# Optimization experiments

Hardware: AMD Instinct MI355X
Metric: run time of the kernel (lower is better)

The kernel has to match this reference:

```python
import jax, jax.numpy as jnp
import numpy as np

NEG_SLOPE = 0.2
EPS = 1e-16

def gatv2(x, edge_index, edge_attr, Wl, bl, We, att, bias):
    """PyG GATv2Conv, heads=1, share_weights=True, with edge_dim."""
    N = x.shape[0]
    h = x @ Wl + bl                      # [N, out] shared lin_l == lin_r
    src, dst = edge_index[0], edge_index[1]
    hj = h[src]                          # source (message) features [E, out]
    hi = h[dst]                          # target features [E, out]
    e = jax.nn.leaky_relu(hi + hj + edge_attr @ We, NEG_SLOPE)  # [E, out]
    score = e @ att                      # [E]
    # segment softmax over edges grouped by destination node
    smax = jax.ops.segment_max(score, dst, num_segments=N)
    ex = jnp.exp(score - smax[dst])
    denom = jax.ops.segment_sum(ex, dst, num_segments=N)
    alpha = ex / (denom[dst] + EPS)      # [E]
    out = jax.ops.segment_sum(hj * alpha[:, None], dst, num_segments=N)
    return out + bias


def setup_inputs() -> dict:
    key = jax.random.key(0)
    N, E = 50000, 800000
    D_IN, D_LAT, D_EDGE, N_ACT = 128, 128, 16, 32
    ks = jax.random.split(key, 16)
    s = 0.05
    inp = {
        "x": jax.random.normal(ks[0], (N, D_IN), jnp.float32),
        "edge_index": jax.random.randint(ks[1], (2, E), 0, N, jnp.int32),
        "edge_attr": jax.random.normal(ks[2], (E, D_EDGE), jnp.float32),
        # gnn_layer: D_IN -> D_LAT
        "Wl1": jax.random.normal(ks[3], (D_IN, D_LAT), jnp.float32) * s,
        "bl1": jnp.zeros((D_LAT,), jnp.float32),
        "We1": jax.random.normal(ks[4], (D_EDGE, D_LAT), jnp.float32) * s,
        "att1": jax.random.normal(ks[5], (D_LAT,), jnp.float32) * s,
        "bias1": jnp.zeros((D_LAT,), jnp.float32),
        # node_layer: D_LAT -> 1
        "Wl2": jax.random.normal(ks[6], (D_LAT, 1), jnp.float32) * s,
        "bl2": jnp.zeros((1,), jnp.float32),
        "We2": jax.random.normal(ks[7], (D_EDGE, 1), jnp.float32) * s,
        "att2": jax.random.normal(ks[8], (1,), jnp.float32) * s,
        "bias2": jnp.zeros((1,), jnp.float32),
        # action_layer: D_LAT -> N_ACT
        "Wl3": jax.random.normal(ks[9], (D_LAT, N_ACT), jnp.float32) * s,
        "bl3": jnp.zeros((N_ACT,), jnp.float32),
        "We3": jax.random.normal(ks[10], (D_EDGE, N_ACT), jnp.float32) * s,
        "att3": jax.random.normal(ks[11], (N_ACT,), jnp.float32) * s,
        "bias3": jnp.zeros((N_ACT,), jnp.float32),
    }
    return inp


def reference(x, edge_index, edge_attr,
              Wl1, bl1, We1, att1, bias1,
              Wl2, bl2, We2, att2, bias2,
              Wl3, bl3, We3, att3, bias3):
    latent = gatv2(x, edge_index, edge_attr, Wl1, bl1, We1, att1, bias1)          # [N, D_LAT]
    node_logits = gatv2(latent, edge_index, edge_attr, Wl2, bl2, We2, att2, bias2)[:, 0]  # [N]
    action_logits = gatv2(latent, edge_index, edge_attr, Wl3, bl3, We3, att3, bias3)      # [N, A]
    # categorical sampling with fixed key (deterministic reference)
    k1, k2 = jax.random.split(jax.random.key(42))
    node_sel = jax.random.categorical(k1, node_logits)
    node_lp = jax.nn.log_softmax(node_logits)[node_sel]
    act_logits_sel = action_logits[node_sel, :]
    action_sel = jax.random.categorical(k2, act_logits_sel)
    action_lp = jax.nn.log_softmax(act_logits_sel)[action_sel]
    return (node_sel, action_sel, node_lp + action_lp)
```

## Files before the change

kernel.cpp:

```cpp
#include <hip/hip_runtime.h>
#include <stdint.h>
#include <math.h>

#define NEG 0.2f
#define TINYF 1.1754943508222875e-38f

typedef float f4 __attribute__((ext_vector_type(4)));
typedef float f2 __attribute__((ext_vector_type(2)));

__host__ __device__ inline void threefry2x32(uint32_t k0, uint32_t k1,
                                             uint32_t x0, uint32_t x1,
                                             uint32_t* o0, uint32_t* o1) {
  uint32_t ks0 = k0, ks1 = k1, ks2 = k0 ^ k1 ^ 0x1BD11BDAu;
  x0 += ks0; x1 += ks1;
#define RR(r) { x0 += x1; x1 = (x1 << (r)) | (x1 >> (32 - (r))); x1 ^= x0; }
  RR(13) RR(15) RR(26) RR(6)
  x0 += ks1; x1 += ks2 + 1u;
  RR(17) RR(29) RR(16) RR(24)
  x0 += ks2; x1 += ks0 + 2u;
  RR(13) RR(15) RR(26) RR(6)
  x0 += ks0; x1 += ks1 + 3u;
  RR(17) RR(29) RR(16) RR(24)
  x0 += ks1; x1 += ks2 + 4u;
  RR(13) RR(15) RR(26) RR(6)
  x0 += ks2; x1 += ks0 + 5u;
#undef RR
  *o0 = x0; *o1 = x1;
}

__device__ inline float gumbel_part(uint32_t ka, uint32_t kb, uint32_t i) {
  uint32_t o0, o1;
  threefry2x32(ka, kb, 0u, i, &o0, &o1);
  uint32_t bits = o0 ^ o1;
  float f = __uint_as_float((bits >> 9) | 0x3f800000u) - 1.0f;
  float u = fmaxf(TINYF, f + TINYF);
  return -logf(-logf(u));
}

__global__ void count_kernel(const int* __restrict__ ei, int E, int* __restrict__ counts) {
  int e = blockIdx.x * blockDim.x + threadIdx.x;
  if (e < E) atomicAdd(&counts[ei[E + e]], 1);
}

#define SCB 256
__global__ __launch_bounds__(256) void scan_partial_kernel(const int* __restrict__ counts,
    int N, int chunk, int* __restrict__ bsum) {
  int b = blockIdx.x;
  int s0 = b * chunk, s1 = s0 + chunk; if (s1 > N) s1 = N;
  int tid = threadIdx.x;
  int v = 0;
  for (int i = s0 + tid; i < s1; i += 256) v += counts[i];
  __shared__ int red[256];
  red[tid] = v; __syncthreads();
  for (int s = 128; s; s >>= 1) { if (tid < s) red[tid] += red[tid + s]; __syncthreads(); }
  if (tid == 0) bsum[b] = red[0];
}

__global__ __launch_bounds__(256) void scan_offsets_kernel(const int* __restrict__ bsum,
    int* __restrict__ boff, int* __restrict__ row_start, int N) {
  int tid = threadIdx.x; int lane = tid & 63; int wv = tid >> 6;
  __shared__ int wsum[4];
  int v = bsum[tid];
  int incl = v;
#pragma unroll
  for (int off = 1; off < 64; off <<= 1) {
    int t = __shfl_up(incl, off);
    if (lane >= off) incl += t;
  }
  if (lane == 63) wsum[wv] = incl;
  __syncthreads();
  if (tid == 0) {
    int s = 0;
    for (int k = 0; k < 4; k++) { int t = wsum[k]; wsum[k] = s; s += t; }
    row_start[N] = s;
  }
  __syncthreads();
  boff[tid] = wsum[wv] + incl - v;
}

__global__ __launch_bounds__(256) void scan_apply_kernel(const int* __restrict__ counts,
    const int* __restrict__ boff, int N, int chunk,
    int* __restrict__ row_start, int* __restrict__ cursor) {
  int b = blockIdx.x;
  int s0 = b * chunk, s1 = s0 + chunk; if (s1 > N) s1 = N;
  int tid = threadIdx.x; int lane = tid & 63; int wv = tid >> 6;
  __shared__ int wsum[4];
  __shared__ int tot_s;
  __shared__ int base_s;
  if (tid == 0) base_s = boff[b];
  __syncthreads();
  for (int c0 = s0; c0 < s1; c0 += 256) {
    int i = c0 + tid;
    int v = (i < s1) ? counts[i] : 0;
    int incl = v;
#pragma unroll
    for (int off = 1; off < 64; off <<= 1) {
      int t = __shfl_up(incl, off);
      if (lane >= off) incl += t;
    }
    if (lane == 63) wsum[wv] = incl;
    __syncthreads();
    if (tid == 0) {
      int s = 0;
      for (int k = 0; k < 4; k++) { int t = wsum[k]; wsum[k] = s; s += t; }
      tot_s = s;
    }
    __syncthreads();
    int base = base_s;
    int excl = base + wsum[wv] + incl - v;
    if (i < s1) { row_start[i] = excl; cursor[i] = excl; }
    __syncthreads();
    if (tid == 0) base_s = base + tot_s;
    __syncthreads();
  }
}

__global__ void scatter_kernel(const int* __restrict__ ei, const float* __restrict__ ea,
                               int E, int* __restrict__ cursor,
                               int* __restrict__ src_csr, float* __restrict__ ea_csr) {
  int e = blockIdx.x * blockDim.x + threadIdx.x;
  if (e < E) {
    int d = ei[E + e];
    int p = atomicAdd(&cursor[d], 1);
    src_csr[p] = ei[e];
    const float4* s4 = (const float4*)&ea[(size_t)e * 16];
    float4* d4 = (float4*)&ea_csr[(size_t)p * 16];
    float4 t0 = s4[0], t1 = s4[1], t2 = s4[2], t3 = s4[3];
    d4[0] = t0; d4[1] = t1; d4[2] = t2; d4[3] = t3;
  }
}

__global__ __launch_bounds__(256) void gemm128_kernel(const float* __restrict__ X,
    const float* __restrict__ W, const float* __restrict__ bias,
    float* __restrict__ out, int M) {
  __shared__ float xs[128][33];
  int row0 = blockIdx.x * 32;
  int tid = threadIdx.x;
  for (int idx = tid; idx < 32 * 128; idx += 256) {
    int r = idx >> 7;
    int k = idx & 127;
    int row = row0 + r;
    xs[k][r] = (row < M) ? X[(size_t)row * 128 + k] : 0.0f;
  }
  __syncthreads();
  int tc = tid & 31, tr = tid >> 5;
  int c0 = tc * 4, r0 = tr * 4;
  float acc[4][4] = {};
#pragma unroll 4
  for (int k = 0; k < 128; k++) {
    float4 w = *(const float4*)&W[k * 128 + c0];
    float x0 = xs[k][r0], x1 = xs[k][r0 + 1], x2 = xs[k][r0 + 2], x3 = xs[k][r0 + 3];
    acc[0][0] += x0 * w.x; acc[0][1] += x0 * w.y; acc[0][2] += x0 * w.z; acc[0][3] += x0 * w.w;
    acc[1][0] += x1 * w.x; acc[1][1] += x1 * w.y; acc[1][2] += x1 * w.z; acc[1][3] += x1 * w.w;
    acc[2][0] += x2 * w.x; acc[2][1] += x2 * w.y; acc[2][2] += x2 * w.z; acc[2][3] += x2 * w.w;
    acc[3][0] += x3 * w.x; acc[3][1] += x3 * w.y; acc[3][2] += x3 * w.z; acc[3][3] += x3 * w.w;
  }
  float4 b4 = *(const float4*)&bias[c0];
  for (int r = 0; r < 4; r++) {
    int row = row0 + r0 + r;
    if (row < M) {
      float4 o;
      o.x = acc[r][0] + b4.x; o.y = acc[r][1] + b4.y;
      o.z = acc[r][2] + b4.z; o.w = acc[r][3] + b4.w;
      *(float4*)&out[(size_t)row * 128 + c0] = o;
    }
  }
}

__global__ __launch_bounds__(256) void gemm32_kernel(const float* __restrict__ X,
    const float* __restrict__ W, const float* __restrict__ bias,
    float* __restrict__ out, int M) {
  int t = blockIdx.x * 256 + threadIdx.x;
  int node = t >> 5, c = t & 31;
  if (node >= M) return;
  const float4* xp = (const float4*)&X[(size_t)node * 128];
  float acc = 0.f;
#pragma unroll
  for (int q = 0; q < 32; q++) {
    float4 x4 = xp[q];
    acc += x4.x * W[(q * 4 + 0) * 32 + c] + x4.y * W[(q * 4 + 1) * 32 + c]
         + x4.z * W[(q * 4 + 2) * 32 + c] + x4.w * W[(q * 4 + 3) * 32 + c];
  }
  out[(size_t)node * 32 + c] = acc + bias[c];
}

__global__ __launch_bounds__(256) void gemv_kernel(const float* __restrict__ X,
    const float* __restrict__ w, const float* __restrict__ b0,
    float* __restrict__ out, int M) {
  int wv = (blockIdx.x * 256 + threadIdx.x) >> 6;
  int lane = threadIdx.x & 63;
  if (wv >= M) return;
  float2 xv = *(const float2*)&X[(size_t)wv * 128 + lane * 2];
  float2 wvv = *(const float2*)&w[lane * 2];
  float v = xv.x * wvv.x + xv.y * wvv.y;
#pragma unroll
  for (int off = 32; off; off >>= 1) v += __shfl_xor(v, off);
  if (lane == 0) out[wv] = v + b0[0];
}

__global__ __launch_bounds__(256) void fused1_kernel(const float* __restrict__ h,
    const int* __restrict__ src_csr, const int* __restrict__ row_start,
    const float* __restrict__ ea_csr,
    const float* __restrict__ We, const float* __restrict__ att,
    const float* __restrict__ bias, float* __restrict__ out, int N) {
  __shared__ float WeS[2048];
  int tid = threadIdx.x;
  for (int i = tid; i < 2048; i += 256) WeS[i] = We[i];
  __syncthreads();
  int hw = (blockIdx.x * 256 + tid) >> 5;
  int lane = tid & 31;
  if (hw >= N) return;
  int c4 = lane * 4;
  const f4* W4 = (const f4*)WeS;
  f4 attv = *(const f4*)&att[c4];
  f4 bb = *(const f4*)&bias[c4];
  int start = row_start[hw];
  int deg = row_start[hw + 1] - start;
  if (deg == 0) {
    *(f4*)&out[(size_t)hw * 128 + c4] = bb;
    return;
  }
  f4 hi = *(const f4*)&h[(size_t)hw * 128 + c4];
  int s_l = (lane < deg) ? src_csr[start + lane] : 0;
  int dcap = deg < 32 ? deg : 32;
  const f4* eap = (const f4*)&ea_csr[(size_t)start * 16];
  float m = -INFINITY, l = 0.f;
  f4 acc = (f4)0.f;
  for (int j = 0; j < deg; j++) {
    int s = (j < dcap) ? __shfl(s_l, j, 32) : src_csr[start + j];
    f4 hj = *(const f4*)&h[(size_t)s * 128 + c4];
    f4 v = hi + hj;
#pragma unroll
    for (int q = 0; q < 4; q++) {
      f4 aq = eap[(size_t)j * 4 + q];
      v += aq.x * W4[(4 * q + 0) * 32 + lane];
      v += aq.y * W4[(4 * q + 1) * 32 + lane];
      v += aq.z * W4[(4 * q + 2) * 32 + lane];
      v += aq.w * W4[(4 * q + 3) * 32 + lane];
    }
    v.x = v.x >= 0.f ? v.x : NEG * v.x;
    v.y = v.y >= 0.f ? v.y : NEG * v.y;
    v.z = v.z >= 0.f ? v.z : NEG * v.z;
    v.w = v.w >= 0.f ? v.w : NEG * v.w;
    f4 pv = v * attv;
    float sc = (pv.x + pv.y) + (pv.z + pv.w);
#pragma unroll
    for (int off = 16; off; off >>= 1) sc += __shfl_xor(sc, off);
    float mn = fmaxf(m, sc);
    float scale = __expf(m - mn);
    float w = __expf(sc - mn);
    l = l * scale + w;
    acc = acc * scale + w * hj;
    m = mn;
  }
  float inv = 1.0f / (l + 1e-16f);
  f4 o = acc * inv + bb;
  *(f4*)&out[(size_t)hw * 128 + c4] = o;
}

__global__ __launch_bounds__(256) void fused23_kernel(
    const float* __restrict__ h3, const float* __restrict__ h2,
    const int* __restrict__ src_csr, const int* __restrict__ row_start,
    const float* __restrict__ ea_csr,
    const float* __restrict__ We3, const float* __restrict__ att3,
    const float* __restrict__ bias3, const float* __restrict__ We2,
    const float* __restrict__ att2, const float* __restrict__ bias2,
    float* __restrict__ out3, float* __restrict__ logits, int N) {
  __shared__ float We3S[512];
  __shared__ float att3S[32];
  __shared__ float We2S[16];
  int tid = threadIdx.x;
  for (int i = tid; i < 512; i += 256) We3S[i] = We3[i];
  if (tid < 32) att3S[tid] = att3[tid];
  if (tid < 16) We2S[tid] = We2[tid];
  __syncthreads();
  int wv = (blockIdx.x * 256 + tid) >> 6;
  int lane = tid & 63;
  if (wv >= N) return;
  int q4 = lane >> 4;
  int l16 = lane & 15;
  int c2 = l16 * 2;
  const f2* W3 = (const f2*)We3S;
  f2 at3 = *(const f2*)&att3S[c2];
  float a2s = att2[0];
  f2 bi3 = *(const f2*)&bias3[c2];
  int start = row_start[wv];
  int deg = row_start[wv + 1] - start;
  if (deg == 0) {
    if (lane < 16) *(f2*)&out3[(size_t)wv * 32 + c2] = bi3;
    if (lane == 0) logits[wv] = bias2[0];
    return;
  }
  f2 hi3 = *(const f2*)&h3[(size_t)wv * 32 + c2];
  float hi2 = h2[wv];
  int s_l = (lane < deg) ? src_csr[start + lane] : 0;
  int dcap = deg < 64 ? deg : 64;
  const float4* eap = (const float4*)&ea_csr[(size_t)start * 16];
  float m3 = -INFINITY, l3 = 0.f; f2 a3 = (f2)0.f;
  float m2 = -INFINITY, l2 = 0.f; float a2 = 0.f;
  for (int j = q4; j < deg; j += 4) {
    int s = (j < dcap) ? __shfl(s_l, j) : src_csr[start + j];
    f2 hj3 = *(const f2*)&h3[(size_t)s * 32 + c2];
    float h2s = h2[s];
    float4 c0 = eap[(size_t)j * 4 + 0];
    float4 c1 = eap[(size_t)j * 4 + 1];
    float4 cc2 = eap[(size_t)j * 4 + 2];
    float4 c3 = eap[(size_t)j * 4 + 3];
    f2 v = hi3 + hj3;
    v += c0.x * W3[0 * 16 + l16];  v += c0.y * W3[1 * 16 + l16];
    v += c0.z * W3[2 * 16 + l16];  v += c0.w * W3[3 * 16 + l16];
    v += c1.x * W3[4 * 16 + l16];  v += c1.y * W3[5 * 16 + l16];
    v += c1.z * W3[6 * 16 + l16];  v += c1.w * W3[7 * 16 + l16];
    v += cc2.x * W3[8 * 16 + l16]; v += cc2.y * W3[9 * 16 + l16];
    v += cc2.z * W3[10 * 16 + l16]; v += cc2.w * W3[11 * 16 + l16];
    v += c3.x * W3[12 * 16 + l16]; v += c3.y * W3[13 * 16 + l16];
    v += c3.z * W3[14 * 16 + l16]; v += c3.w * W3[15 * 16 + l16];
    v.x = v.x >= 0.f ? v.x : NEG * v.x;
    v.y = v.y >= 0.f ? v.y : NEG * v.y;
    float t3 = v.x * at3.x + v.y * at3.y;
#pragma unroll
    for (int off = 8; off; off >>= 1) t3 += __shfl_xor(t3, off);
    float v2 = hi2 + h2s;
    v2 += c0.x * We2S[0]  + c0.y * We2S[1]  + c0.z * We2S[2]  + c0.w * We2S[3];
    v2 += c1.x * We2S[4]  + c1.y * We2S[5]  + c1.z * We2S[6]  + c1.w * We2S[7];
    v2 += cc2.x * We2S[8] + cc2.y * We2S[9] + cc2.z * We2S[10] + cc2.w * We2S[11];
    v2 += c3.x * We2S[12] + c3.y * We2S[13] + c3.z * We2S[14] + c3.w * We2S[15];
    v2 = v2 >= 0.f ? v2 : NEG * v2;
    float t2 = v2 * a2s;
    float mn3 = fmaxf(m3, t3);
    float sc3 = __expf(m3 - mn3);
    float w3 = __expf(t3 - mn3);
    l3 = l3 * sc3 + w3;
    a3 = a3 * sc3 + w3 * hj3;
    m3 = mn3;
    float mn2 = fmaxf(m2, t2);
    float sc2 = __expf(m2 - mn2);
    float w2 = __expf(t2 - mn2);
    l2 = l2 * sc2 + w2;
    a2 = a2 * sc2 + w2 * h2s;
    m2 = mn2;
  }
#pragma unroll
  for (int off = 16; off <= 32; off <<= 1) {
    float m3o = __shfl_xor(m3, off), l3o = __shfl_xor(l3, off);
    float ax = __shfl_xor(a3.x, off), ay = __shfl_xor(a3.y, off);
    float M3 = fmaxf(m3, m3o);
    float sA = (m3 == -INFINITY) ? 0.f : __expf(m3 - M3);
    float sB = (m3o == -INFINITY) ? 0.f : __expf(m3o - M3);
    l3 = l3 * sA + l3o * sB;
    a3.x = a3.x * sA + ax * sB;
    a3.y = a3.y * sA + ay * sB;
    m3 = M3;
    float m2o = __shfl_xor(m2, off), l2o = __shfl_xor(l2, off);
    float az = __shfl_xor(a2, off);
    float M2 = fmaxf(m2, m2o);
    float tA = (m2 == -INFINITY) ? 0.f : __expf(m2 - M2);
    float tB = (m2o == -INFINITY) ? 0.f : __expf(m2o - M2);
    l2 = l2 * tA + l2o * tB;
    a2 = a2 * tA + az * tB;
    m2 = M2;
  }
  if (lane < 16) {
    f2 o;
    o.x = a3.x / (l3 + 1e-16f) + bi3.x;
    o.y = a3.y / (l3 + 1e-16f) + bi3.y;
    *(f2*)&out3[(size_t)wv * 32 + c2] = o;
  }
  if (lane == 0) logits[wv] = a2 / (l2 + 1e-16f) + bias2[0];
}

#define NSB 64
__global__ __launch_bounds__(256) void node_partial_kernel(const float* __restrict__ logits,
    int N, uint32_t ka, uint32_t kb,
    float* __restrict__ pB, int* __restrict__ pI,
    float* __restrict__ pM, float* __restrict__ pL) {
  int chunk = (N + NSB - 1) / NSB;
  int s0 = blockIdx.x * chunk;
  int s1 = s0 + chunk; if (s1 > N) s1 = N;
  int tid = threadIdx.x;
  float best = -INFINITY; int bi = 0x7fffffff;
  float m = -INFINITY, l = 0.f;
  for (int i = s0 + tid; i < s1; i += 256) {
    float lg = logits[i];
    float mn = fmaxf(m, lg);
    l = l * __expf(m - mn) + __expf(lg - mn);
    m = mn;
    float v = lg + gumbel_part(ka, kb, (uint32_t)i);
    if (v > best) { best = v; bi = i; }
  }
  __shared__ float sb[256], sm[256], sl[256];
  __shared__ int si[256];
  sb[tid] = best; si[tid] = bi; sm[tid] = m; sl[tid] = l;
  __syncthreads();
  for (int s = 128; s; s >>= 1) {
    if (tid < s) {
      if (sb[tid + s] > sb[tid] || (sb[tid + s] == sb[tid] && si[tid + s] < si[tid])) {
        sb[tid] = sb[tid + s]; si[tid] = si[tid + s];
      }
      float M = fmaxf(sm[tid], sm[tid + s]);
      float t0 = (sm[tid] == -INFINITY) ? 0.f : sl[tid] * __expf(sm[tid] - M);
      float t1 = (sm[tid + s] == -INFINITY) ? 0.f : sl[tid + s] * __expf(sm[tid + s] - M);
      sm[tid] = M; sl[tid] = t0 + t1;
    }
    __syncthreads();
  }
  if (tid == 0) { pB[blockIdx.x] = sb[0]; pI[blockIdx.x] = si[0]; pM[blockIdx.x] = sm[0]; pL[blockIdx.x] = sl[0]; }
}

__global__ __launch_bounds__(64) void node_final_kernel(const float* __restrict__ logits,
    const float* __restrict__ pB, const int* __restrict__ pI,
    const float* __restrict__ pM, const float* __restrict__ pL,
    float* __restrict__ scal) {
  int lane = threadIdx.x;
  float best = pB[lane]; int bi = pI[lane];
  float m = pM[lane]; float l = pL[lane];
#pragma unroll
  for (int off = 32; off; off >>= 1) {
    float ob = __shfl_xor(best, off); int oi = __shfl_xor(bi, off);
    if (ob > best || (ob == best && oi < bi)) { best = ob; bi = oi; }
    float om = __shfl_xor(m, off); float ol = __shfl_xor(l, off);
    float M = fmaxf(m, om);
    float t0 = (m == -INFINITY) ? 0.f : l * __expf(m - M);
    float t1 = (om == -INFINITY) ? 0.f : ol * __expf(om - M);
    m = M; l = t0 + t1;
  }
  if (lane == 0) {
    ((int*)scal)[0] = bi;
    scal[3] = logits[bi] - (m + logf(l));
  }
}

__global__ __launch_bounds__(64) void action_kernel(const float* __restrict__ out3,
    const float* __restrict__ scal, uint32_t ka, uint32_t kb,
    float* __restrict__ dout, int out_size) {
  int lane = threadIdx.x;
  int sel = ((const int*)scal)[0];
  float v = -INFINITY, noisy = -INFINITY;
  if (lane < 32) {
    v = out3[(size_t)sel * 32 + lane];
    noisy = v + gumbel_part(ka, kb, (uint32_t)lane);
  }
  int idx = lane;
  float nv = noisy;
#pragma unroll
  for (int off = 32; off; off >>= 1) {
    float ov = __shfl_xor(nv, off);
    int oi = __shfl_xor(idx, off);
    if (ov > nv || (ov == nv && oi < idx)) { nv = ov; idx = oi; }
  }
  float vm = v;
#pragma unroll
  for (int off = 32; off; off >>= 1) vm = fmaxf(vm, __shfl_xor(vm, off));
  float ex = (lane < 32) ? expf(v - vm) : 0.f;
#pragma unroll
  for (int off = 32; off; off >>= 1) ex += __shfl_xor(ex, off);
  float vsel = __shfl(v, idx);
  if (lane == 0) {
    float action_lp = vsel - vm - logf(ex);
    dout[0] = (float)sel;
    dout[1] = (float)idx;
    dout[2] = scal[3] + action_lp;
  }
  for (int i = 3 + lane; i < out_size; i += 64) dout[i] = 0.f;
}

extern "C" void kernel_launch(void* const* d_in, const int* in_sizes, int n_in,
                              void* d_out, int out_size, void* d_ws, size_t ws_size,
                              hipStream_t stream) {
  const float* x     = (const float*)d_in[0];
  const int*   ei    = (const int*)d_in[1];
  const float* ea    = (const float*)d_in[2];
  const float* Wl1   = (const float*)d_in[3];
  const float* bl1   = (const float*)d_in[4];
  const float* We1   = (const float*)d_in[5];
  const float* att1  = (const float*)d_in[6];
  const float* bias1 = (const float*)d_in[7];
  const float* Wl2   = (const float*)d_in[8];
  const float* bl2   = (const float*)d_in[9];
  const float* We2   = (const float*)d_in[10];
  const float* att2  = (const float*)d_in[11];
  const float* bias2 = (const float*)d_in[12];
  const float* Wl3   = (const float*)d_in[13];
  const float* bl3   = (const float*)d_in[14];
  const float* We3   = (const float*)d_in[15];
  const float* att3  = (const float*)d_in[16];
  const float* bias3 = (const float*)d_in[17];
  int N = in_sizes[0] / 128;
  int E = in_sizes[1] / 2;
  float* out = (float*)d_out;

  char* p = (char*)d_ws;
  auto alloc = [&](size_t bytes) -> char* {
    char* r = p; p += (bytes + 255) & ~(size_t)255; return r;
  };
  float* h1      = (float*)alloc((size_t)N * 128 * 4);
  float* latent  = (float*)alloc((size_t)N * 128 * 4);
  float* h3      = (float*)alloc((size_t)N * 32 * 4);
  float* h2      = (float*)alloc((size_t)N * 4);
  float* logits  = (float*)alloc((size_t)N * 4);
  float* out3    = (float*)alloc((size_t)N * 32 * 4);
  int* counts    = (int*)alloc((size_t)N * 4);
  int* row_start = (int*)alloc((size_t)(N + 1) * 4);
  int* cursor    = (int*)alloc((size_t)N * 4);
  int* src_csr   = (int*)alloc((size_t)E * 4);
  float* ea_csr  = (float*)alloc((size_t)E * 16 * 4);
  int* bsum      = (int*)alloc(SCB * 4);
  int* boff      = (int*)alloc(SCB * 4);
  float* pB      = (float*)alloc(NSB * 4);
  int*   pI      = (int*)alloc(NSB * 4);
  float* pM      = (float*)alloc(NSB * 4);
  float* pL      = (float*)alloc(NSB * 4);
  float* scal    = (float*)alloc(64);
  (void)ws_size; (void)n_in;

  uint32_t k1a, k1b, k2a, k2b;
  threefry2x32(0u, 42u, 0u, 0u, &k1a, &k1b);
  threefry2x32(0u, 42u, 0u, 1u, &k2a, &k2b);

  int chunk = (N + SCB - 1) / SCB;

  hipMemsetAsync(counts, 0, (size_t)N * 4, stream);
  count_kernel<<<(E + 255) / 256, 256, 0, stream>>>(ei, E, counts);
  scan_partial_kernel<<<SCB, 256, 0, stream>>>(counts, N, chunk, bsum);
  scan_offsets_kernel<<<1, 256, 0, stream>>>(bsum, boff, row_start, N);
  scan_apply_kernel<<<SCB, 256, 0, stream>>>(counts, boff, N, chunk, row_start, cursor);
  scatter_kernel<<<(E + 255) / 256, 256, 0, stream>>>(ei, ea, E, cursor, src_csr, ea_csr);

  gemm128_kernel<<<(N + 31) / 32, 256, 0, stream>>>(x, Wl1, bl1, h1, N);
  fused1_kernel<<<(N + 7) / 8, 256, 0, stream>>>(h1, src_csr, row_start,
                                                 ea_csr, We1, att1, bias1, latent, N);

  gemm32_kernel<<<((size_t)N * 32 + 255) / 256, 256, 0, stream>>>(latent, Wl3, bl3, h3, N);
  gemv_kernel<<<(N + 3) / 4, 256, 0, stream>>>(latent, Wl2, bl2, h2, N);

  fused23_kernel<<<(N + 3) / 4, 256, 0, stream>>>(h3, h2, src_csr, row_start, ea_csr,
                                                  We3, att3, bias3, We2, att2, bias2,
                                                  out3, logits, N);

  node_partial_kernel<<<NSB, 256, 0, stream>>>(logits, N, k1a, k1b, pB, pI, pM, pL);
  node_final_kernel<<<1, 64, 0, stream>>>(logits, pB, pI, pM, pL, scal);
  action_kernel<<<1, 64, 0, stream>>>(out3, scal, k2a, k2b, out, out_size);
}
```

Baseline: 584.6 us.

## Batch four edges per step in fused1 and interleave h3/h2 into one buffer

The layer-1 fused kernel now processes four edges per iteration. It loads the four source feature vectors up front, reuses each shared-memory We row across the four edges, and does one online-softmax rescale per group of four. This is meant to add memory-level parallelism for the random gathers and to cut LDS reads and serial shuffle-reduction latency. Separately, the h3 (32 floats) and h2 (1 float) outputs are packed into a single 40-float-stride buffer, so the gather in fused23 hits one row instead of two arrays. This costs more registers per thread and some padding bandwidth.

```diff
diff --git a/kernel.cpp b/kernel.cpp
--- a/kernel.cpp
+++ b/kernel.cpp
@@ -169,7 +169,7 @@
 
 __global__ __launch_bounds__(256) void gemm32_kernel(const float* __restrict__ X,
     const float* __restrict__ W, const float* __restrict__ bias,
-    float* __restrict__ out, int M) {
+    float* __restrict__ ch, int M) {
   int t = blockIdx.x * 256 + threadIdx.x;
   int node = t >> 5, c = t & 31;
   if (node >= M) return;
@@ -181,12 +181,12 @@
     acc += x4.x * W[(q * 4 + 0) * 32 + c] + x4.y * W[(q * 4 + 1) * 32 + c]
          + x4.z * W[(q * 4 + 2) * 32 + c] + x4.w * W[(q * 4 + 3) * 32 + c];
   }
-  out[(size_t)node * 32 + c] = acc + bias[c];
+  ch[(size_t)node * 40 + c] = acc + bias[c];
 }
 
 __global__ __launch_bounds__(256) void gemv_kernel(const float* __restrict__ X,
     const float* __restrict__ w, const float* __restrict__ b0,
-    float* __restrict__ out, int M) {
+    float* __restrict__ ch, int M) {
   int wv = (blockIdx.x * 256 + threadIdx.x) >> 6;
   int lane = threadIdx.x & 63;
   if (wv >= M) return;
@@ -195,7 +195,7 @@
   float v = xv.x * wvv.x + xv.y * wvv.y;
 #pragma unroll
   for (int off = 32; off; off >>= 1) v += __shfl_xor(v, off);
-  if (lane == 0) out[wv] = v + b0[0];
+  if (lane == 0) ch[(size_t)wv * 40 + 32] = v + b0[0];
 }
 
 __global__ __launch_bounds__(256) void fused1_kernel(const float* __restrict__ h,
@@ -226,31 +226,70 @@
   const f4* eap = (const f4*)&ea_csr[(size_t)start * 16];
   float m = -INFINITY, l = 0.f;
   f4 acc = (f4)0.f;
-  for (int j = 0; j < deg; j++) {
-    int s = (j < dcap) ? __shfl(s_l, j, 32) : src_csr[start + j];
-    f4 hj = *(const f4*)&h[(size_t)s * 128 + c4];
-    f4 v = hi + hj;
-#pragma unroll
-    for (int q = 0; q < 4; q++) {
-      f4 aq = eap[(size_t)j * 4 + q];
-      v += aq.x * W4[(4 * q + 0) * 32 + lane];
-      v += aq.y * W4[(4 * q + 1) * 32 + lane];
-      v += aq.z * W4[(4 * q + 2) * 32 + lane];
-      v += aq.w * W4[(4 * q + 3) * 32 + lane];
-    }
-    v.x = v.x >= 0.f ? v.x : NEG * v.x;
-    v.y = v.y >= 0.f ? v.y : NEG * v.y;
-    v.z = v.z >= 0.f ? v.z : NEG * v.z;
-    v.w = v.w >= 0.f ? v.w : NEG * v.w;
-    f4 pv = v * attv;
-    float sc = (pv.x + pv.y) + (pv.z + pv.w);
-#pragma unroll
-    for (int off = 16; off; off >>= 1) sc += __shfl_xor(sc, off);
-    float mn = fmaxf(m, sc);
+  for (int j0 = 0; j0 < deg; j0 += 4) {
+    f4 hj[4];
+    int jc[4];
+#pragma unroll
+    for (int t = 0; t < 4; t++) {
+      int j = j0 + t;
+      jc[t] = (j < deg) ? j : j0;
+      int s = (jc[t] < dcap) ? __shfl(s_l, jc[t], 32) : src_csr[start + jc[t]];
+      hj[t] = *(const f4*)&h[(size_t)s * 128 + c4];
+    }
+    f4 vb0 = (f4)0.f, vb1 = (f4)0.f, vb2 = (f4)0.f, vb3 = (f4)0.f;
+#pragma unroll
+    for (int kc = 0; kc < 4; kc++) {
+      f4 w0 = W4[(4 * kc + 0) * 32 + lane];
+      f4 w1 = W4[(4 * kc + 1) * 32 + lane];
+      f4 w2 = W4[(4 * kc + 2) * 32 + lane];
+      f4 w3 = W4[(4 * kc + 3) * 32 + lane];
+      {
+        f4 aq = eap[(size_t)jc[0] * 4 + kc];
+        vb0 += aq.x * w0 + aq.y * w1 + aq.z * w2 + aq.w * w3;
+      }
+      {
+        f4 aq = eap[(size_t)jc[1] * 4 + kc];
+        vb1 += aq.x * w0 + aq.y * w1 + aq.z * w2 + aq.w * w3;
+      }
+      {
+        f4 aq = eap[(size_t)jc[2] * 4 + kc];
+        vb2 += aq.x * w0 + aq.y * w1 + aq.z * w2 + aq.w * w3;
+      }
+      {
+        f4 aq = eap[(size_t)jc[3] * 4 + kc];
+        vb3 += aq.x * w0 + aq.y * w1 + aq.z * w2 + aq.w * w3;
+      }
+    }
+    float sc[4];
+#pragma unroll
+    for (int t = 0; t < 4; t++) {
+      f4 v = (t == 0 ? vb0 : t == 1 ? vb1 : t == 2 ? vb2 : vb3) + hi + hj[t];
+      v.x = v.x >= 0.f ? v.x : NEG * v.x;
+      v.y = v.y >= 0.f ? v.y : NEG * v.y;
+      v.z = v.z >= 0.f ? v.z : NEG * v.z;
+      v.w = v.w >= 0.f ? v.w : NEG * v.w;
+      f4 pv = v * attv;
+      sc[t] = (pv.x + pv.y) + (pv.z + pv.w);
+    }
+#pragma unroll
+    for (int off = 16; off; off >>= 1) {
+      sc[0] += __shfl_xor(sc[0], off);
+      sc[1] += __shfl_xor(sc[1], off);
+      sc[2] += __shfl_xor(sc[2], off);
+      sc[3] += __shfl_xor(sc[3], off);
+    }
+    if (j0 + 1 >= deg) sc[1] = -INFINITY;
+    if (j0 + 2 >= deg) sc[2] = -INFINITY;
+    if (j0 + 3 >= deg) sc[3] = -INFINITY;
+    float mb = fmaxf(fmaxf(sc[0], sc[1]), fmaxf(sc[2], sc[3]));
+    float mn = fmaxf(m, mb);
     float scale = __expf(m - mn);
-    float w = __expf(sc - mn);
-    l = l * scale + w;
-    acc = acc * scale + w * hj;
+    float w0 = __expf(sc[0] - mn);
+    float w1 = __expf(sc[1] - mn);
+    float w2 = __expf(sc[2] - mn);
+    float w3 = __expf(sc[3] - mn);
+    l = l * scale + ((w0 + w1) + (w2 + w3));
+    acc = acc * scale + w0 * hj[0] + w1 * hj[1] + w2 * hj[2] + w3 * hj[3];
     m = mn;
   }
   float inv = 1.0f / (l + 1e-16f);
@@ -259,7 +298,7 @@
 }
 
 __global__ __launch_bounds__(256) void fused23_kernel(
-    const float* __restrict__ h3, const float* __restrict__ h2,
+    const float* __restrict__ ch,
     const int* __restrict__ src_csr, const int* __restrict__ row_start,
     const float* __restrict__ ea_csr,
     const float* __restrict__ We3, const float* __restrict__ att3,
@@ -291,8 +330,8 @@
     if (lane == 0) logits[wv] = bias2[0];
     return;
   }
-  f2 hi3 = *(const f2*)&h3[(size_t)wv * 32 + c2];
-  float hi2 = h2[wv];
+  f2 hi3 = *(const f2*)&ch[(size_t)wv * 40 + c2];
+  float hi2 = ch[(size_t)wv * 40 + 32];
   int s_l = (lane < deg) ? src_csr[start + lane] : 0;
   int dcap = deg < 64 ? deg : 64;
   const float4* eap = (const float4*)&ea_csr[(size_t)start * 16];
@@ -300,8 +339,8 @@
   float m2 = -INFINITY, l2 = 0.f; float a2 = 0.f;
   for (int j = q4; j < deg; j += 4) {
     int s = (j < dcap) ? __shfl(s_l, j) : src_csr[start + j];
-    f2 hj3 = *(const f2*)&h3[(size_t)s * 32 + c2];
-    float h2s = h2[s];
+    f2 hj3 = *(const f2*)&ch[(size_t)s * 40 + c2];
+    float h2s = ch[(size_t)s * 40 + 32];
     float4 c0 = eap[(size_t)j * 4 + 0];
     float4 c1 = eap[(size_t)j * 4 + 1];
     float4 cc2 = eap[(size_t)j * 4 + 2];
@@ -495,8 +534,7 @@
   };
   float* h1      = (float*)alloc((size_t)N * 128 * 4);
   float* latent  = (float*)alloc((size_t)N * 128 * 4);
-  float* h3      = (float*)alloc((size_t)N * 32 * 4);
-  float* h2      = (float*)alloc((size_t)N * 4);
+  float* ch      = (float*)alloc((size_t)N * 40 * 4);
   float* logits  = (float*)alloc((size_t)N * 4);
   float* out3    = (float*)alloc((size_t)N * 32 * 4);
   int* counts    = (int*)alloc((size_t)N * 4);
@@ -530,10 +568,10 @@
   fused1_kernel<<<(N + 7) / 8, 256, 0, stream>>>(h1, src_csr, row_start,
                                                  ea_csr, We1, att1, bias1, latent, N);
 
-  gemm32_kernel<<<((size_t)N * 32 + 255) / 256, 256, 0, stream>>>(latent, Wl3, bl3, h3, N);
-  gemv_kernel<<<(N + 3) / 4, 256, 0, stream>>>(latent, Wl2, bl2, h2, N);
-
-  fused23_kernel<<<(N + 3) / 4, 256, 0, stream>>>(h3, h2, src_csr, row_start, ea_csr,
+  gemm32_kernel<<<((size_t)N * 32 + 255) / 256, 256, 0, stream>>>(latent, Wl3, bl3, ch, N);
+  gemv_kernel<<<(N + 3) / 4, 256, 0, stream>>>(latent, Wl2, bl2, ch, N);
+
+  fused23_kernel<<<(N + 3) / 4, 256, 0, stream>>>(ch, src_csr, row_start, ea_csr,
                                                   We3, att3, bias3, We2, att2, bias2,
                                                   out3, logits, N);
 
```

Measured after the change: 711.4 us. 21.7% more time.

## Split layer-1 into edge-parallel score pass and node-parallel aggregation

Applied to the files above, without the earlier changes.

The fused online-softmax layer-1 kernel is replaced by two kernels. The first computes edge scores in an edge-parallel grid-stride loop, with We held in registers and a new dst_csr array. The second does a two-pass softmax per node and gathers with four gathers in flight per iteration. Separately, h3 and h2 are packed into one 40-float-stride buffer so fused23 reads one array. The split removes the serial per-edge dependency chain and degree imbalance, at the cost of an extra score array, an extra dst array, and re-reading h rows in both passes.

```diff
diff --git a/kernel.cpp b/kernel.cpp
--- a/kernel.cpp
+++ b/kernel.cpp
@@ -117,12 +117,14 @@
 
 __global__ void scatter_kernel(const int* __restrict__ ei, const float* __restrict__ ea,
                                int E, int* __restrict__ cursor,
-                               int* __restrict__ src_csr, float* __restrict__ ea_csr) {
+                               int* __restrict__ src_csr, int* __restrict__ dst_csr,
+                               float* __restrict__ ea_csr) {
   int e = blockIdx.x * blockDim.x + threadIdx.x;
   if (e < E) {
     int d = ei[E + e];
     int p = atomicAdd(&cursor[d], 1);
     src_csr[p] = ei[e];
+    dst_csr[p] = d;
     const float4* s4 = (const float4*)&ea[(size_t)e * 16];
     float4* d4 = (float4*)&ea_csr[(size_t)p * 16];
     float4 t0 = s4[0], t1 = s4[1], t2 = s4[2], t3 = s4[3];
@@ -169,7 +171,7 @@
 
 __global__ __launch_bounds__(256) void gemm32_kernel(const float* __restrict__ X,
     const float* __restrict__ W, const float* __restrict__ bias,
-    float* __restrict__ out, int M) {
+    float* __restrict__ ch, int M) {
   int t = blockIdx.x * 256 + threadIdx.x;
   int node = t >> 5, c = t & 31;
   if (node >= M) return;
@@ -181,12 +183,12 @@
     acc += x4.x * W[(q * 4 + 0) * 32 + c] + x4.y * W[(q * 4 + 1) * 32 + c]
          + x4.z * W[(q * 4 + 2) * 32 + c] + x4.w * W[(q * 4 + 3) * 32 + c];
   }
-  out[(size_t)node * 32 + c] = acc + bias[c];
+  ch[(size_t)node * 40 + c] = acc + bias[c];
 }
 
 __global__ __launch_bounds__(256) void gemv_kernel(const float* __restrict__ X,
     const float* __restrict__ w, const float* __restrict__ b0,
-    float* __restrict__ out, int M) {
+    float* __restrict__ ch, int M) {
   int wv = (blockIdx.x * 256 + threadIdx.x) >> 6;
   int lane = threadIdx.x & 63;
   if (wv >= M) return;
@@ -195,24 +197,56 @@
   float v = xv.x * wvv.x + xv.y * wvv.y;
 #pragma unroll
   for (int off = 32; off; off >>= 1) v += __shfl_xor(v, off);
-  if (lane == 0) out[wv] = v + b0[0];
-}
-
-__global__ __launch_bounds__(256) void fused1_kernel(const float* __restrict__ h,
-    const int* __restrict__ src_csr, const int* __restrict__ row_start,
+  if (lane == 0) ch[(size_t)wv * 40 + 32] = v + b0[0];
+}
+
+__global__ __launch_bounds__(256) void escore1_kernel(const float* __restrict__ h,
+    const int* __restrict__ src_csr, const int* __restrict__ dst_csr,
     const float* __restrict__ ea_csr,
     const float* __restrict__ We, const float* __restrict__ att,
-    const float* __restrict__ bias, float* __restrict__ out, int N) {
-  __shared__ float WeS[2048];
+    float* __restrict__ score, int E) {
   int tid = threadIdx.x;
-  for (int i = tid; i < 2048; i += 256) WeS[i] = We[i];
-  __syncthreads();
+  int lane = tid & 31;
+  int c4 = lane * 4;
+  f4 we[16];
+#pragma unroll
+  for (int k = 0; k < 16; k++) we[k] = *(const f4*)&We[k * 128 + c4];
+  f4 attv = *(const f4*)&att[c4];
+  int hw0 = (blockIdx.x * 256 + tid) >> 5;
+  int hwTot = (gridDim.x * 256) >> 5;
+  for (int p = hw0; p < E; p += hwTot) {
+    int s = src_csr[p];
+    int d = dst_csr[p];
+    f4 hi = *(const f4*)&h[(size_t)d * 128 + c4];
+    f4 hj = *(const f4*)&h[(size_t)s * 128 + c4];
+    const f4* eap = (const f4*)&ea_csr[(size_t)p * 16];
+    f4 a0 = eap[0], a1 = eap[1], a2 = eap[2], a3 = eap[3];
+    f4 v = hi + hj;
+    v += a0.x * we[0];  v += a0.y * we[1];  v += a0.z * we[2];  v += a0.w * we[3];
+    v += a1.x * we[4];  v += a1.y * we[5];  v += a1.z * we[6];  v += a1.w * we[7];
+    v += a2.x * we[8];  v += a2.y * we[9];  v += a2.z * we[10]; v += a2.w * we[11];
+    v += a3.x * we[12]; v += a3.y * we[13]; v += a3.z * we[14]; v += a3.w * we[15];
+    v.x = v.x >= 0.f ? v.x : NEG * v.x;
+    v.y = v.y >= 0.f ? v.y : NEG * v.y;
+    v.z = v.z >= 0.f ? v.z : NEG * v.z;
+    v.w = v.w >= 0.f ? v.w : NEG * v.w;
+    f4 pv = v * attv;
+    float sc = (pv.x + pv.y) + (pv.z + pv.w);
+#pragma unroll
+    for (int off = 16; off; off >>= 1) sc += __shfl_xor(sc, off);
+    if (lane == 0) score[p] = sc;
+  }
+}
+
+__global__ __launch_bounds__(256) void agg1_kernel(const float* __restrict__ h,
+    const int* __restrict__ src_csr, const int* __restrict__ row_start,
+    const float* __restrict__ score, const float* __restrict__ bias,
+    float* __restrict__ out, int N) {
+  int tid = threadIdx.x;
   int hw = (blockIdx.x * 256 + tid) >> 5;
   int lane = tid & 31;
   if (hw >= N) return;
   int c4 = lane * 4;
-  const f4* W4 = (const f4*)WeS;
-  f4 attv = *(const f4*)&att[c4];
   f4 bb = *(const f4*)&bias[c4];
   int start = row_start[hw];
   int deg = row_start[hw + 1] - start;
@@ -220,46 +254,43 @@
     *(f4*)&out[(size_t)hw * 128 + c4] = bb;
     return;
   }
-  f4 hi = *(const f4*)&h[(size_t)hw * 128 + c4];
-  int s_l = (lane < deg) ? src_csr[start + lane] : 0;
+  float mx = -INFINITY;
+  for (int j = lane; j < deg; j += 32) mx = fmaxf(mx, score[start + j]);
+#pragma unroll
+  for (int off = 16; off; off >>= 1) mx = fmaxf(mx, __shfl_xor(mx, off));
+  float se = 0.f;
+  for (int j = lane; j < deg; j += 32) se += __expf(score[start + j] - mx);
+#pragma unroll
+  for (int off = 16; off; off >>= 1) se += __shfl_xor(se, off);
+  float inv = 1.0f / (se + 1e-16f);
+  float w_l = 0.f; int s_l = 0;
+  if (lane < deg) {
+    w_l = __expf(score[start + lane] - mx) * inv;
+    s_l = src_csr[start + lane];
+  }
   int dcap = deg < 32 ? deg : 32;
-  const f4* eap = (const f4*)&ea_csr[(size_t)start * 16];
-  float m = -INFINITY, l = 0.f;
   f4 acc = (f4)0.f;
-  for (int j = 0; j < deg; j++) {
-    int s = (j < dcap) ? __shfl(s_l, j, 32) : src_csr[start + j];
-    f4 hj = *(const f4*)&h[(size_t)s * 128 + c4];
-    f4 v = hi + hj;
-#pragma unroll
-    for (int q = 0; q < 4; q++) {
-      f4 aq = eap[(size_t)j * 4 + q];
-      v += aq.x * W4[(4 * q + 0) * 32 + lane];
-      v += aq.y * W4[(4 * q + 1) * 32 + lane];
-      v += aq.z * W4[(4 * q + 2) * 32 + lane];
-      v += aq.w * W4[(4 * q + 3) * 32 + lane];
+  for (int j0 = 0; j0 < deg; j0 += 4) {
+    f4 hj[4]; float w[4];
+#pragma unroll
+    for (int t = 0; t < 4; t++) {
+      int j = j0 + t;
+      bool valid = (j < deg);
+      int jc = valid ? j : j0;
+      int s; float wt;
+      if (jc < dcap) { s = __shfl(s_l, jc, 32); wt = __shfl(w_l, jc, 32); }
+      else { s = src_csr[start + jc]; wt = __expf(score[start + jc] - mx) * inv; }
+      w[t] = valid ? wt : 0.f;
+      hj[t] = *(const f4*)&h[(size_t)s * 128 + c4];
     }
-    v.x = v.x >= 0.f ? v.x : NEG * v.x;
-    v.y = v.y >= 0.f ? v.y : NEG * v.y;
-    v.z = v.z >= 0.f ? v.z : NEG * v.z;
-    v.w = v.w >= 0.f ? v.w : NEG * v.w;
-    f4 pv = v * attv;
-    float sc = (pv.x + pv.y) + (pv.z + pv.w);
-#pragma unroll
-    for (int off = 16; off; off >>= 1) sc += __shfl_xor(sc, off);
-    float mn = fmaxf(m, sc);
-    float scale = __expf(m - mn);
-    float w = __expf(sc - mn);
-    l = l * scale + w;
-    acc = acc * scale + w * hj;
-    m = mn;
-  }
-  float inv = 1.0f / (l + 1e-16f);
-  f4 o = acc * inv + bb;
+    acc += w[0] * hj[0] + w[1] * hj[1] + w[2] * hj[2] + w[3] * hj[3];
+  }
+  f4 o = acc + bb;
   *(f4*)&out[(size_t)hw * 128 + c4] = o;
 }
 
 __global__ __launch_bounds__(256) void fused23_kernel(
-    const float* __restrict__ h3, const float* __restrict__ h2,
+    const float* __restrict__ ch,
     const int* __restrict__ src_csr, const int* __restrict__ row_start,
     const float* __restrict__ ea_csr,
     const float* __restrict__ We3, const float* __restrict__ att3,
@@ -291,8 +322,8 @@
     if (lane == 0) logits[wv] = bias2[0];
     return;
   }
-  f2 hi3 = *(const f2*)&h3[(size_t)wv * 32 + c2];
-  float hi2 = h2[wv];
+  f2 hi3 = *(const f2*)&ch[(size_t)wv * 40 + c2];
+  float hi2 = ch[(size_t)wv * 40 + 32];
   int s_l = (lane < deg) ? src_csr[start + lane] : 0;
   int dcap = deg < 64 ? deg : 64;
   const float4* eap = (const float4*)&ea_csr[(size_t)start * 16];
@@ -300,8 +331,8 @@
   float m2 = -INFINITY, l2 = 0.f; float a2 = 0.f;
   for (int j = q4; j < deg; j += 4) {
     int s = (j < dcap) ? __shfl(s_l, j) : src_csr[start + j];
-    f2 hj3 = *(const f2*)&h3[(size_t)s * 32 + c2];
-    float h2s = h2[s];
+    f2 hj3 = *(const f2*)&ch[(size_t)s * 40 + c2];
+    float h2s = ch[(size_t)s * 40 + 32];
     float4 c0 = eap[(size_t)j * 4 + 0];
     float4 c1 = eap[(size_t)j * 4 + 1];
     float4 cc2 = eap[(size_t)j * 4 + 2];
@@ -495,15 +526,16 @@
   };
   float* h1      = (float*)alloc((size_t)N * 128 * 4);
   float* latent  = (float*)alloc((size_t)N * 128 * 4);
-  float* h3      = (float*)alloc((size_t)N * 32 * 4);
-  float* h2      = (float*)alloc((size_t)N * 4);
+  float* ch      = (float*)alloc((size_t)N * 40 * 4);
   float* logits  = (float*)alloc((size_t)N * 4);
   float* out3    = (float*)alloc((size_t)N * 32 * 4);
   int* counts    = (int*)alloc((size_t)N * 4);
   int* row_start = (int*)alloc((size_t)(N + 1) * 4);
   int* cursor    = (int*)alloc((size_t)N * 4);
   int* src_csr   = (int*)alloc((size_t)E * 4);
+  int* dst_csr   = (int*)alloc((size_t)E * 4);
   float* ea_csr  = (float*)alloc((size_t)E * 16 * 4);
+  float* score   = (float*)alloc((size_t)E * 4);
   int* bsum      = (int*)alloc(SCB * 4);
   int* boff      = (int*)alloc(SCB * 4);
   float* pB      = (float*)alloc(NSB * 4);
@@ -524,16 +556,19 @@
   scan_partial_kernel<<<SCB, 256, 0, stream>>>(counts, N, chunk, bsum);
   scan_offsets_kernel<<<1, 256, 0, stream>>>(bsum, boff, row_start, N);
   scan_apply_kernel<<<SCB, 256, 0, stream>>>(counts, boff, N, chunk, row_start, cursor);
-  scatter_kernel<<<(E + 255) / 256, 256, 0, stream>>>(ei, ea, E, cursor, src_csr, ea_csr);
+  scatter_kernel<<<(E + 255) / 256, 256, 0, stream>>>(ei, ea, E, cursor,
+                                                      src_csr, dst_csr, ea_csr);
 
   gemm128_kernel<<<(N + 31) / 32, 256, 0, stream>>>(x, Wl1, bl1, h1, N);
-  fused1_kernel<<<(N + 7) / 8, 256, 0, stream>>>(h1, src_csr, row_start,
-                                                 ea_csr, We1, att1, bias1, latent, N);
-
-  gemm32_kernel<<<((size_t)N * 32 + 255) / 256, 256, 0, stream>>>(latent, Wl3, bl3, h3, N);
-  gemv_kernel<<<(N + 3) / 4, 256, 0, stream>>>(latent, Wl2, bl2, h2, N);
-
-  fused23_kernel<<<(N + 3) / 4, 256, 0, stream>>>(h3, h2, src_csr, row_start, ea_csr,
+  escore1_kernel<<<2048, 256, 0, stream>>>(h1, src_csr, dst_csr, ea_csr,
+                                           We1, att1, score, E);
+  agg1_kernel<<<(N + 7) / 8, 256, 0, stream>>>(h1, src_csr, row_start, score,
+                                               bias1, latent, N);
+
+  gemm32_kernel<<<((size_t)N * 32 + 255) / 256, 256, 0, stream>>>(latent, Wl3, bl3, ch, N);
+  gemv_kernel<<<(N + 3) / 4, 256, 0, stream>>>(latent, Wl2, bl2, ch, N);
+
+  fused23_kernel<<<(N + 3) / 4, 256, 0, stream>>>(ch, src_csr, row_start, ea_csr,
                                                   We3, att3, bias3, We2, att2, bias2,
                                                   out3, logits, N);
 
```

Result: slower. 681.8 us (+16.6%).
